# Optimization experiments

Hardware: AMD Instinct MI355X
Metric: run time of the kernel (lower is better)

The kernel has to match this reference:

```python
import jax, jax.numpy as jnp
import numpy as np


def setup_inputs() -> dict:
    key = jax.random.key(0)
    k1, k2, k3, k4, k5 = jax.random.split(key, 5)
    B, T, C = 64, 1024, 768
    scale = 1.0 / np.sqrt(C)
    tokens = jax.random.normal(k1, (B, T, C), dtype=jnp.float32)
    mask_topk = jax.random.randint(k2, (B, T), 0, 2) > 0
    Wq = jax.random.normal(k3, (C, C), dtype=jnp.float32) * scale
    Wk = jax.random.normal(k4, (C, C), dtype=jnp.float32) * scale
    Wv = jax.random.normal(k5, (C, C), dtype=jnp.float32) * scale
    return {"tokens": tokens, "mask_topk": mask_topk, "Wq": Wq, "Wk": Wk, "Wv": Wv}


def reference(tokens, mask_topk, Wq, Wk, Wv):
    # tokens: [B, T, C]; mask_topk: [B, T] bool; W*: [C, C] (torch Linear weight, y = x @ W.T)
    C = tokens.shape[-1]
    m = mask_topk.astype(tokens.dtype)                      # [B, T]
    cnt = jnp.sum(m, axis=-1, keepdims=True)                # [B, 1]
    masked_sum = jnp.einsum('btc,bt->bc', tokens, m)        # [B, C]
    mean_all = jnp.mean(tokens, axis=1)                     # fallback when mask is empty
    q_sal = jnp.where(cnt > 0, masked_sum / jnp.maximum(cnt, 1.0), mean_all)  # [B, C]
    q_sal = q_sal[:, None, :]                               # [B, 1, C]

    Q = jnp.einsum('bqc,dc->bqd', q_sal, Wq)                # [B, 1, C]
    K = jnp.einsum('btc,dc->btd', tokens, Wk)               # [B, T, C]
    V = jnp.einsum('btc,dc->btd', tokens, Wv)               # [B, T, C]

    scores = jnp.einsum('bqd,btd->bqt', Q, K) / jnp.sqrt(jnp.asarray(C, tokens.dtype))
    attn = jax.nn.softmax(scores, axis=-1)                  # [B, 1, T]
    v_fg = jnp.einsum('bqt,btd->bqd', attn, V)[:, 0, :]     # [B, C]
    return (v_fg, attn)
```

## Files before the change

### kernel.cpp

```cpp
#include <hip/hip_runtime.h>
#include <hip/hip_bf16.h>

#define B 64
#define T 1024
#define C 768
#define TSPLIT 32
#define TCHUNK (T / TSPLIT)

#define OFF_MSUM   64
#define OFF_ASUM   (OFF_MSUM + B*TSPLIT*C)
#define OFF_QSAL   (OFF_ASUM + B*TSPLIT*C)
#define OFF_Q      (OFF_QSAL + B*C)
#define OFF_QK     (OFF_Q + B*C)
#define OFF_SCORES (OFF_QK + B*C)
#define OFF_MPART  (OFF_SCORES + B*T)
#define OFF_SPART  (OFF_MPART + B*TSPLIT)
#define OFF_COEF   (OFF_SPART + B*TSPLIT)
#define OFF_PPART  (OFF_COEF + B*TSPLIT)
#define OFF_POOLED (OFF_PPART + B*TSPLIT*C)

__device__ __forceinline__ bool read_mask(const void* mask, int mode, int idx) {
    if (mode == 1) return ((const unsigned char*)mask)[idx] != 0;
    if (mode == 2) return ((const float*)mask)[idx] != 0.0f;
    return ((const int*)mask)[idx] != 0;
}

__global__ void k_detect(const void* mask, int* mode_out) {
    __shared__ int s_not01, s_isf;
    int tid = threadIdx.x;
    if (tid == 0) { s_not01 = 0; s_isf = 0; }
    __syncthreads();
    const int* mi = (const int*)mask;
    int not01 = 0, isf = 0;
    for (int k = 0; k < 64; ++k) {
        int v = mi[tid + 256 * k];
        if (v != 0 && v != 1) not01 = 1;
        if (v == 0x3F800000) isf = 1;
    }
    if (not01) atomicOr(&s_not01, 1);
    if (isf)   atomicOr(&s_isf, 1);
    __syncthreads();
    if (tid == 0) *mode_out = s_isf ? 2 : (s_not01 ? 1 : 0);
}

__global__ void k_partial_sums(const float* __restrict__ tokens, const void* mask,
                               const int* modep, float* __restrict__ msum,
                               float* __restrict__ asum) {
    int ts = blockIdx.x, b = blockIdx.y, tid = threadIdx.x;
    int mode = *modep;
    __shared__ float s_m[TCHUNK];
    if (tid < TCHUNK)
        s_m[tid] = read_mask(mask, mode, b * T + ts * TCHUNK + tid) ? 1.f : 0.f;
    __syncthreads();
    int c = tid * 4;
    float4 ms = {0, 0, 0, 0}, as = {0, 0, 0, 0};
    const float* tb = tokens + (size_t)b * T * C;
#pragma unroll 4
    for (int r = 0; r < TCHUNK; ++r) {
        int t = ts * TCHUNK + r;
        float4 x = *(const float4*)(tb + (size_t)t * C + c);
        as.x += x.x; as.y += x.y; as.z += x.z; as.w += x.w;
        float wm = s_m[r];
        ms.x += wm * x.x; ms.y += wm * x.y; ms.z += wm * x.z; ms.w += wm * x.w;
    }
    size_t o = (size_t)(b * TSPLIT + ts) * C + c;
    *(float4*)(msum + o) = ms;
    *(float4*)(asum + o) = as;
}

__global__ void k_qsal(const void* mask, const int* modep,
                       const float* __restrict__ msum, const float* __restrict__ asum,
                       float* __restrict__ qsal) {
    int b = blockIdx.x, tid = threadIdx.x;
    int mode = *modep;
    __shared__ float red[256];
    float cnt0 = 0.f;
    for (int t = tid; t < T; t += 256)
        cnt0 += read_mask(mask, mode, b * T + t) ? 1.f : 0.f;
    red[tid] = cnt0;
    __syncthreads();
    for (int s = 128; s > 0; s >>= 1) {
        if (tid < s) red[tid] += red[tid + s];
        __syncthreads();
    }
    float cnt = red[0];
    float scale = (cnt > 0.f) ? (1.f / fmaxf(cnt, 1.f)) : (1.f / (float)T);
    bool use_masked = (cnt > 0.f);
    for (int c = tid; c < C; c += 256) {
        float m = 0.f, a = 0.f;
#pragma unroll 8
        for (int p = 0; p < TSPLIT; ++p) {
            m += msum[(size_t)(b * TSPLIT + p) * C + c];
            a += asum[(size_t)(b * TSPLIT + p) * C + c];
        }
        qsal[b * C + c] = (use_masked ? m : a) * scale;
    }
}

__global__ void k_rowdot4(const float* __restrict__ vin, const float* __restrict__ W,
                          float* __restrict__ vout, float scale) {
    int tid = threadIdx.x;
    int gid = blockIdx.x * 64 + (tid >> 2);
    int sub = tid & 3;
    int b = gid / C, d = gid - b * C;
    const float4* v = (const float4*)(vin + (size_t)b * C);
    const float4* w = (const float4*)(W + (size_t)d * C);
    float acc = 0.f;
    int j0 = sub * 48;
#pragma unroll 8
    for (int j = j0; j < j0 + 48; ++j) {
        float4 a = v[j], x = w[j];
        acc += a.x * x.x + a.y * x.y + a.z * x.z + a.w * x.w;
    }
    acc += __shfl_xor(acc, 1);
    acc += __shfl_xor(acc, 2);
    if (sub == 0) vout[gid] = acc * scale;
}

__global__ void k_coldot4(const float* __restrict__ Q, const float* __restrict__ Wk,
                          float* __restrict__ qk) {
    int tid = threadIdx.x;
    int gid = blockIdx.x * 64 + (tid >> 2);
    int sub = tid & 3;
    int b = gid / C, c = gid - b * C;
    const float* Qb = Q + (size_t)b * C;
    float acc = 0.f;
    int d0 = sub * 192;
#pragma unroll 8
    for (int i = 0; i < 192; ++i) {
        int d = d0 + i;
        acc += Qb[d] * Wk[(size_t)d * C + c];
    }
    acc += __shfl_xor(acc, 1);
    acc += __shfl_xor(acc, 2);
    if (sub == 0) qk[gid] = acc * 0.03608439182435161f;
}

__global__ void k_fused(const float* __restrict__ tokens, const float* __restrict__ qk,
                        float* __restrict__ scores, float* __restrict__ mpart,
                        float* __restrict__ spart, float* __restrict__ ppart) {
    __shared__ float sq[C];
    __shared__ float ssc[TCHUNK];
    __shared__ float sw[TCHUNK];
    int ts = blockIdx.x, b = blockIdx.y, tid = threadIdx.x;
    ((float4*)sq)[tid] = ((const float4*)(qk + (size_t)b * C))[tid];
    __syncthreads();
    int wave = tid >> 6, lane = tid & 63;
    const float* tb = tokens + (size_t)b * T * C;
    const float4* q4 = (const float4*)sq;
    for (int r = wave; r < TCHUNK; r += 3) {
        int t = ts * TCHUNK + r;
        const float4* row = (const float4*)(tb + (size_t)t * C);
        float acc = 0.f;
#pragma unroll
        for (int j = 0; j < 3; ++j) {
            int idx = lane + 64 * j;
            float4 x = row[idx], q = q4[idx];
            acc += x.x * q.x + x.y * q.y + x.z * q.z + x.w * q.w;
        }
        for (int s = 32; s > 0; s >>= 1) acc += __shfl_xor(acc, s);
        if (lane == 0) { ssc[r] = acc; scores[(size_t)b * T + t] = acc; }
    }
    __syncthreads();
    float m = -3.4e38f;
#pragma unroll
    for (int r = 0; r < TCHUNK; ++r) m = fmaxf(m, ssc[r]);
    if (tid < TCHUNK) sw[tid] = expf(ssc[tid] - m);
    __syncthreads();
    float s = 0.f;
#pragma unroll
    for (int r = 0; r < TCHUNK; ++r) s += sw[r];
    int c = tid * 4;
    float4 acc = {0, 0, 0, 0};
#pragma unroll 4
    for (int r = 0; r < TCHUNK; ++r) {
        int t = ts * TCHUNK + r;
        float wv = sw[r];
        float4 x = *(const float4*)(tb + (size_t)t * C + c);
        acc.x += wv * x.x; acc.y += wv * x.y; acc.z += wv * x.z; acc.w += wv * x.w;
    }
    *(float4*)(ppart + (size_t)(b * TSPLIT + ts) * C + c) = acc;
    if (tid == 0) { mpart[b * TSPLIT + ts] = m; spart[b * TSPLIT + ts] = s; }
}

__global__ void k_combine(const float* __restrict__ scores, const float* __restrict__ mpart,
                          const float* __restrict__ spart, float* __restrict__ coef,
                          float* __restrict__ attn) {
    int b = blockIdx.x, tid = threadIdx.x;
    __shared__ float sm[TSPLIT], ss[TSPLIT];
    if (tid < TSPLIT) { sm[tid] = mpart[b * TSPLIT + tid]; ss[tid] = spart[b * TSPLIT + tid]; }
    __syncthreads();
    float M = -3.4e38f;
#pragma unroll
    for (int p = 0; p < TSPLIT; ++p) M = fmaxf(M, sm[p]);
    float Z = 0.f;
#pragma unroll
    for (int p = 0; p < TSPLIT; ++p) Z += ss[p] * expf(sm[p] - M);
    float invZ = 1.f / Z;
    if (tid < TSPLIT) coef[b * TSPLIT + tid] = expf(sm[tid] - M) * invZ;
    float4 sc = ((const float4*)(scores + (size_t)b * T))[tid];
    float4 o;
    o.x = expf(sc.x - M) * invZ; o.y = expf(sc.y - M) * invZ;
    o.z = expf(sc.z - M) * invZ; o.w = expf(sc.w - M) * invZ;
    ((float4*)(attn + (size_t)b * T))[tid] = o;
}

__global__ void k_pool_reduce(const float* __restrict__ ppart, const float* __restrict__ coef,
                              float* __restrict__ pooled) {
    int gid = blockIdx.x * 256 + threadIdx.x;
    int b = gid / C, c = gid - b * C;
    float a = 0.f;
#pragma unroll 8
    for (int p = 0; p < TSPLIT; ++p)
        a += coef[b * TSPLIT + p] * ppart[(size_t)(b * TSPLIT + p) * C + c];
    pooled[gid] = a;
}

extern "C" void kernel_launch(void* const* d_in, const int* in_sizes, int n_in,
                              void* d_out, int out_size, void* d_ws, size_t ws_size,
                              hipStream_t stream) {
    const float* tokens = (const float*)d_in[0];
    const void*  mask   = d_in[1];
    const float* Wq     = (const float*)d_in[2];
    const float* Wk     = (const float*)d_in[3];
    const float* Wv     = (const float*)d_in[4];

    float* ws     = (float*)d_ws;
    int*   mode   = (int*)d_ws;
    float* msum   = ws + OFF_MSUM;
    float* asum   = ws + OFF_ASUM;
    float* qsal   = ws + OFF_QSAL;
    float* Qv     = ws + OFF_Q;
    float* qk     = ws + OFF_QK;
    float* scores = ws + OFF_SCORES;
    float* mpart  = ws + OFF_MPART;
    float* spart  = ws + OFF_SPART;
    float* coef   = ws + OFF_COEF;
    float* ppart  = ws + OFF_PPART;
    float* pooled = ws + OFF_POOLED;

    float* v_fg = (float*)d_out;
    float* attn = (float*)d_out + B * C;

    k_detect<<<1, 256, 0, stream>>>(mask, mode);
    k_partial_sums<<<dim3(TSPLIT, B), 192, 0, stream>>>(tokens, mask, mode, msum, asum);
    k_qsal<<<B, 256, 0, stream>>>(mask, mode, msum, asum, qsal);
    k_rowdot4<<<(B * C) / 64, 256, 0, stream>>>(qsal, Wq, Qv, 1.0f);
    k_coldot4<<<(B * C) / 64, 256, 0, stream>>>(Qv, Wk, qk);
    k_fused<<<dim3(TSPLIT, B), 192, 0, stream>>>(tokens, qk, scores, mpart, spart, ppart);
    k_combine<<<B, 256, 0, stream>>>(scores, mpart, spart, coef, attn);
    k_pool_reduce<<<(B * C) / 256, 256, 0, stream>>>(ppart, coef, pooled);
    k_rowdot4<<<(B * C) / 64, 256, 0, stream>>>(pooled, Wv, v_fg, 1.0f);
}
```

Before: 214.0 us.

## Fuse qsal reduction into Wq matvec and pool reduction into Wv matvec

Computes the per-chunk mask counts inside the first pass, then merges the q_sal reduction with the Wq row-dot and the coefficient-weighted pool reduction with the Wv row-dot. Each batch vector is staged in shared memory, and the Q vector is also staged in shared memory for the Wk column-dot. This cuts the launch count from 9 to 7 and removes the qsal, coef and pooled round-trips through global memory. In exchange, each of the 12 column blocks per batch now redoes the TSPLIT-way partial reduction, so the msum/asum/ppart partial reads are multiplied by 12.

```diff
diff --git a/kernel.cpp b/kernel.cpp
--- a/kernel.cpp
+++ b/kernel.cpp
@@ -9,15 +9,13 @@
 
 #define OFF_MSUM   64
 #define OFF_ASUM   (OFF_MSUM + B*TSPLIT*C)
-#define OFF_QSAL   (OFF_ASUM + B*TSPLIT*C)
-#define OFF_Q      (OFF_QSAL + B*C)
+#define OFF_CNT    (OFF_ASUM + B*TSPLIT*C)
+#define OFF_Q      (OFF_CNT + B*TSPLIT)
 #define OFF_QK     (OFF_Q + B*C)
 #define OFF_SCORES (OFF_QK + B*C)
 #define OFF_MPART  (OFF_SCORES + B*T)
 #define OFF_SPART  (OFF_MPART + B*TSPLIT)
-#define OFF_COEF   (OFF_SPART + B*TSPLIT)
-#define OFF_PPART  (OFF_COEF + B*TSPLIT)
-#define OFF_POOLED (OFF_PPART + B*TSPLIT*C)
+#define OFF_PPART  (OFF_SPART + B*TSPLIT)
 
 __device__ __forceinline__ bool read_mask(const void* mask, int mode, int idx) {
     if (mode == 1) return ((const unsigned char*)mask)[idx] != 0;
@@ -43,9 +41,9 @@
     if (tid == 0) *mode_out = s_isf ? 2 : (s_not01 ? 1 : 0);
 }
 
-__global__ void k_partial_sums(const float* __restrict__ tokens, const void* mask,
-                               const int* modep, float* __restrict__ msum,
-                               float* __restrict__ asum) {
+__global__ __launch_bounds__(192) void
+k_pass1(const float* __restrict__ tokens, const void* mask, const int* modep,
+        float* __restrict__ msum, float* __restrict__ asum, float* __restrict__ cntpart) {
     int ts = blockIdx.x, b = blockIdx.y, tid = threadIdx.x;
     int mode = *modep;
     __shared__ float s_m[TCHUNK];
@@ -66,79 +64,70 @@
     size_t o = (size_t)(b * TSPLIT + ts) * C + c;
     *(float4*)(msum + o) = ms;
     *(float4*)(asum + o) = as;
-}
-
-__global__ void k_qsal(const void* mask, const int* modep,
-                       const float* __restrict__ msum, const float* __restrict__ asum,
-                       float* __restrict__ qsal) {
-    int b = blockIdx.x, tid = threadIdx.x;
-    int mode = *modep;
-    __shared__ float red[256];
-    float cnt0 = 0.f;
-    for (int t = tid; t < T; t += 256)
-        cnt0 += read_mask(mask, mode, b * T + t) ? 1.f : 0.f;
-    red[tid] = cnt0;
-    __syncthreads();
-    for (int s = 128; s > 0; s >>= 1) {
-        if (tid < s) red[tid] += red[tid + s];
-        __syncthreads();
-    }
-    float cnt = red[0];
-    float scale = (cnt > 0.f) ? (1.f / fmaxf(cnt, 1.f)) : (1.f / (float)T);
-    bool use_masked = (cnt > 0.f);
+    if (tid == 0) {
+        float cnt = 0.f;
+#pragma unroll
+        for (int r = 0; r < TCHUNK; ++r) cnt += s_m[r];
+        cntpart[b * TSPLIT + ts] = cnt;
+    }
+}
+
+__global__ __launch_bounds__(256) void
+k_qsal_rowdot(const float* __restrict__ msum, const float* __restrict__ asum,
+              const float* __restrict__ cntpart, const float* __restrict__ Wq,
+              float* __restrict__ Qv) {
+    int b = blockIdx.y, tid = threadIdx.x;
+    __shared__ float sq[C];
+    float cnt = 0.f;
+#pragma unroll
+    for (int p = 0; p < TSPLIT; ++p) cnt += cntpart[b * TSPLIT + p];
+    bool um = (cnt > 0.f);
+    float scale = um ? (1.f / fmaxf(cnt, 1.f)) : (1.f / (float)T);
+    const float* src = um ? msum : asum;
     for (int c = tid; c < C; c += 256) {
-        float m = 0.f, a = 0.f;
-#pragma unroll 8
-        for (int p = 0; p < TSPLIT; ++p) {
-            m += msum[(size_t)(b * TSPLIT + p) * C + c];
-            a += asum[(size_t)(b * TSPLIT + p) * C + c];
-        }
-        qsal[b * C + c] = (use_masked ? m : a) * scale;
-    }
-}
-
-__global__ void k_rowdot4(const float* __restrict__ vin, const float* __restrict__ W,
-                          float* __restrict__ vout, float scale) {
-    int tid = threadIdx.x;
-    int gid = blockIdx.x * 64 + (tid >> 2);
-    int sub = tid & 3;
-    int b = gid / C, d = gid - b * C;
-    const float4* v = (const float4*)(vin + (size_t)b * C);
-    const float4* w = (const float4*)(W + (size_t)d * C);
+        float a = 0.f;
+#pragma unroll 8
+        for (int p = 0; p < TSPLIT; ++p) a += src[(size_t)(b * TSPLIT + p) * C + c];
+        sq[c] = a * scale;
+    }
+    __syncthreads();
+    int d = blockIdx.x * 64 + (tid >> 2), sub = tid & 3;
+    const float4* w = (const float4*)(Wq + (size_t)d * C);
+    const float4* v4 = (const float4*)sq;
     float acc = 0.f;
-    int j0 = sub * 48;
-#pragma unroll 8
-    for (int j = j0; j < j0 + 48; ++j) {
-        float4 a = v[j], x = w[j];
+#pragma unroll 8
+    for (int j = sub * 48; j < sub * 48 + 48; ++j) {
+        float4 a = v4[j], x = w[j];
         acc += a.x * x.x + a.y * x.y + a.z * x.z + a.w * x.w;
     }
     acc += __shfl_xor(acc, 1);
     acc += __shfl_xor(acc, 2);
-    if (sub == 0) vout[gid] = acc * scale;
-}
-
-__global__ void k_coldot4(const float* __restrict__ Q, const float* __restrict__ Wk,
-                          float* __restrict__ qk) {
-    int tid = threadIdx.x;
-    int gid = blockIdx.x * 64 + (tid >> 2);
-    int sub = tid & 3;
-    int b = gid / C, c = gid - b * C;
-    const float* Qb = Q + (size_t)b * C;
+    if (sub == 0) Qv[b * C + d] = acc;
+}
+
+__global__ __launch_bounds__(256) void
+k_coldot(const float* __restrict__ Qv, const float* __restrict__ Wk,
+         float* __restrict__ qk) {
+    int b = blockIdx.y, tid = threadIdx.x;
+    __shared__ float sQ[C];
+    for (int c = tid; c < C; c += 256) sQ[c] = Qv[b * C + c];
+    __syncthreads();
+    int c = blockIdx.x * 64 + (tid >> 2), sub = tid & 3;
     float acc = 0.f;
-    int d0 = sub * 192;
 #pragma unroll 8
     for (int i = 0; i < 192; ++i) {
-        int d = d0 + i;
-        acc += Qb[d] * Wk[(size_t)d * C + c];
+        int d = sub * 192 + i;
+        acc += sQ[d] * Wk[(size_t)d * C + c];
     }
     acc += __shfl_xor(acc, 1);
     acc += __shfl_xor(acc, 2);
-    if (sub == 0) qk[gid] = acc * 0.03608439182435161f;
-}
-
-__global__ void k_fused(const float* __restrict__ tokens, const float* __restrict__ qk,
-                        float* __restrict__ scores, float* __restrict__ mpart,
-                        float* __restrict__ spart, float* __restrict__ ppart) {
+    if (sub == 0) qk[b * C + c] = acc * 0.03608439182435161f;
+}
+
+__global__ __launch_bounds__(192) void
+k_fused(const float* __restrict__ tokens, const float* __restrict__ qk,
+        float* __restrict__ scores, float* __restrict__ mpart,
+        float* __restrict__ spart, float* __restrict__ ppart) {
     __shared__ float sq[C];
     __shared__ float ssc[TCHUNK];
     __shared__ float sw[TCHUNK];
@@ -183,21 +172,17 @@
     if (tid == 0) { mpart[b * TSPLIT + ts] = m; spart[b * TSPLIT + ts] = s; }
 }
 
-__global__ void k_combine(const float* __restrict__ scores, const float* __restrict__ mpart,
-                          const float* __restrict__ spart, float* __restrict__ coef,
-                          float* __restrict__ attn) {
+__global__ __launch_bounds__(256) void
+k_attn(const float* __restrict__ scores, const float* __restrict__ mpart,
+       const float* __restrict__ spart, float* __restrict__ attn) {
     int b = blockIdx.x, tid = threadIdx.x;
-    __shared__ float sm[TSPLIT], ss[TSPLIT];
-    if (tid < TSPLIT) { sm[tid] = mpart[b * TSPLIT + tid]; ss[tid] = spart[b * TSPLIT + tid]; }
-    __syncthreads();
     float M = -3.4e38f;
 #pragma unroll
-    for (int p = 0; p < TSPLIT; ++p) M = fmaxf(M, sm[p]);
+    for (int p = 0; p < TSPLIT; ++p) M = fmaxf(M, mpart[b * TSPLIT + p]);
     float Z = 0.f;
 #pragma unroll
-    for (int p = 0; p < TSPLIT; ++p) Z += ss[p] * expf(sm[p] - M);
+    for (int p = 0; p < TSPLIT; ++p) Z += spart[b * TSPLIT + p] * expf(mpart[b * TSPLIT + p] - M);
     float invZ = 1.f / Z;
-    if (tid < TSPLIT) coef[b * TSPLIT + tid] = expf(sm[tid] - M) * invZ;
     float4 sc = ((const float4*)(scores + (size_t)b * T))[tid];
     float4 o;
     o.x = expf(sc.x - M) * invZ; o.y = expf(sc.y - M) * invZ;
@@ -205,15 +190,42 @@
     ((float4*)(attn + (size_t)b * T))[tid] = o;
 }
 
-__global__ void k_pool_reduce(const float* __restrict__ ppart, const float* __restrict__ coef,
-                              float* __restrict__ pooled) {
-    int gid = blockIdx.x * 256 + threadIdx.x;
-    int b = gid / C, c = gid - b * C;
-    float a = 0.f;
-#pragma unroll 8
-    for (int p = 0; p < TSPLIT; ++p)
-        a += coef[b * TSPLIT + p] * ppart[(size_t)(b * TSPLIT + p) * C + c];
-    pooled[gid] = a;
+__global__ __launch_bounds__(256) void
+k_vfg(const float* __restrict__ ppart, const float* __restrict__ mpart,
+      const float* __restrict__ spart, const float* __restrict__ Wv,
+      float* __restrict__ vfg) {
+    int b = blockIdx.y, tid = threadIdx.x;
+    __shared__ float sp[C];
+    float M = -3.4e38f;
+#pragma unroll
+    for (int p = 0; p < TSPLIT; ++p) M = fmaxf(M, mpart[b * TSPLIT + p]);
+    float Z = 0.f;
+#pragma unroll
+    for (int p = 0; p < TSPLIT; ++p) Z += spart[b * TSPLIT + p] * expf(mpart[b * TSPLIT + p] - M);
+    float invZ = 1.f / Z;
+    float coef[TSPLIT];
+#pragma unroll
+    for (int p = 0; p < TSPLIT; ++p) coef[p] = expf(mpart[b * TSPLIT + p] - M) * invZ;
+    for (int c = tid; c < C; c += 256) {
+        float a = 0.f;
+#pragma unroll 8
+        for (int p = 0; p < TSPLIT; ++p)
+            a += coef[p] * ppart[(size_t)(b * TSPLIT + p) * C + c];
+        sp[c] = a;
+    }
+    __syncthreads();
+    int d = blockIdx.x * 64 + (tid >> 2), sub = tid & 3;
+    const float4* w = (const float4*)(Wv + (size_t)d * C);
+    const float4* v4 = (const float4*)sp;
+    float acc = 0.f;
+#pragma unroll 8
+    for (int j = sub * 48; j < sub * 48 + 48; ++j) {
+        float4 a = v4[j], x = w[j];
+        acc += a.x * x.x + a.y * x.y + a.z * x.z + a.w * x.w;
+    }
+    acc += __shfl_xor(acc, 1);
+    acc += __shfl_xor(acc, 2);
+    if (sub == 0) vfg[b * C + d] = acc;
 }
 
 extern "C" void kernel_launch(void* const* d_in, const int* in_sizes, int n_in,
@@ -225,30 +237,26 @@
     const float* Wk     = (const float*)d_in[3];
     const float* Wv     = (const float*)d_in[4];
 
-    float* ws     = (float*)d_ws;
-    int*   mode   = (int*)d_ws;
-    float* msum   = ws + OFF_MSUM;
-    float* asum   = ws + OFF_ASUM;
-    float* qsal   = ws + OFF_QSAL;
-    float* Qv     = ws + OFF_Q;
-    float* qk     = ws + OFF_QK;
-    float* scores = ws + OFF_SCORES;
-    float* mpart  = ws + OFF_MPART;
-    float* spart  = ws + OFF_SPART;
-    float* coef   = ws + OFF_COEF;
-    float* ppart  = ws + OFF_PPART;
-    float* pooled = ws + OFF_POOLED;
+    float* ws      = (float*)d_ws;
+    int*   mode    = (int*)d_ws;
+    float* msum    = ws + OFF_MSUM;
+    float* asum    = ws + OFF_ASUM;
+    float* cntpart = ws + OFF_CNT;
+    float* Qv      = ws + OFF_Q;
+    float* qk      = ws + OFF_QK;
+    float* scores  = ws + OFF_SCORES;
+    float* mpart   = ws + OFF_MPART;
+    float* spart   = ws + OFF_SPART;
+    float* ppart   = ws + OFF_PPART;
 
     float* v_fg = (float*)d_out;
     float* attn = (float*)d_out + B * C;
 
     k_detect<<<1, 256, 0, stream>>>(mask, mode);
-    k_partial_sums<<<dim3(TSPLIT, B), 192, 0, stream>>>(tokens, mask, mode, msum, asum);
-    k_qsal<<<B, 256, 0, stream>>>(mask, mode, msum, asum, qsal);
-    k_rowdot4<<<(B * C) / 64, 256, 0, stream>>>(qsal, Wq, Qv, 1.0f);
-    k_coldot4<<<(B * C) / 64, 256, 0, stream>>>(Qv, Wk, qk);
+    k_pass1<<<dim3(TSPLIT, B), 192, 0, stream>>>(tokens, mask, mode, msum, asum, cntpart);
+    k_qsal_rowdot<<<dim3(12, B), 256, 0, stream>>>(msum, asum, cntpart, Wq, Qv);
+    k_coldot<<<dim3(12, B), 256, 0, stream>>>(Qv, Wk, qk);
     k_fused<<<dim3(TSPLIT, B), 192, 0, stream>>>(tokens, qk, scores, mpart, spart, ppart);
-    k_combine<<<B, 256, 0, stream>>>(scores, mpart, spart, coef, attn);
-    k_pool_reduce<<<(B * C) / 256, 256, 0, stream>>>(ppart, coef, pooled);
-    k_rowdot4<<<(B * C) / 64, 256, 0, stream>>>(pooled, Wv, v_fg, 1.0f);
-}
+    k_attn<<<B, 256, 0, stream>>>(scores, mpart, spart, attn);
+    k_vfg<<<dim3(12, B), 256, 0, stream>>>(ppart, mpart, spart, Wv, v_fg);
+}
```

Measured after the change: 172.4 us. 19.4% less time.
